# Optimization experiments

Hardware: AMD Instinct MI355X
Metric: run time of the kernel (lower is better)

Reference implementation:

```python
import jax, jax.numpy as jnp
import numpy as np

N_NODES = 50000
N_EDGES = 1600000


def gcn_conv(x, edge_index, W, b):
    """PyG GCNConv: linear transform, add self-loops, symmetric deg^-1/2 norm, scatter-add."""
    n = x.shape[0]
    h = x @ W  # [N, out]
    loop = jnp.arange(n)
    src = jnp.concatenate([edge_index[0], loop])
    dst = jnp.concatenate([edge_index[1], loop])
    ones = jnp.ones(src.shape[0], dtype=h.dtype)
    deg = jax.ops.segment_sum(ones, dst, num_segments=n)  # in-degree incl. self-loop
    dinv = jnp.where(deg > 0, jax.lax.rsqrt(deg), 0.0)
    norm = dinv[src] * dinv[dst]  # [E+N]
    msg = h[src] * norm[:, None]  # gathered, normalized messages
    out = jax.ops.segment_sum(msg, dst, num_segments=n)
    return out + b


def setup_inputs() -> dict:
    key = jax.random.key(0)
    k1, k2, k3, k4 = jax.random.split(key, 4)
    x = jax.random.normal(k1, (N_NODES, 512), dtype=jnp.float32)
    edge_index = jax.random.randint(k2, (2, N_EDGES), 0, N_NODES, dtype=jnp.int64)
    W1 = jax.random.normal(k3, (512, 128), dtype=jnp.float32) * (1.0 / np.sqrt(512))
    b1 = jnp.zeros((128,), dtype=jnp.float32)
    W2 = jax.random.normal(k4, (128, 40), dtype=jnp.float32) * (1.0 / np.sqrt(128))
    b2 = jnp.zeros((40,), dtype=jnp.float32)
    return {"x": x, "edge_index": edge_index, "W1": W1, "b1": b1, "W2": W2, "b2": b2}


def reference(x, edge_index, W1, b1, W2, b2):
    h = gcn_conv(x, edge_index, W1, b1)
    h = jax.nn.relu(h)
    h = gcn_conv(h, edge_index, W2, b2)
    return jax.nn.log_softmax(h, axis=1)
```

## Files before the change

kernel.cpp:

```cpp
#include <hip/hip_runtime.h>
#include <hip/hip_bf16.h>
#include <math.h>


#define FEAT1 512
#define FEAT2 128
#define FEAT3 40

typedef __attribute__((ext_vector_type(8))) short bf16x8;
typedef __attribute__((ext_vector_type(4))) float f32x4;

__device__ __forceinline__ unsigned short f2bf(float f) {
    union { float f; unsigned u; } c; c.f = f;
    unsigned r = c.u + 0x7fff + ((c.u >> 16) & 1);
    return (unsigned short)(r >> 16);
}
__device__ __forceinline__ float bf2f(unsigned v16) {
    union { unsigned u; float f; } c; c.u = v16 << 16;
    return c.f;
}

__global__ void detect_i64_kernel(const int* __restrict__ ei, int* flagp) {
    __shared__ int any;
    if (threadIdx.x == 0) any = 0;
    __syncthreads();
    int v = ei[2 * threadIdx.x + 1];
    if (v != 0) any = 1;
    __syncthreads();
    if (threadIdx.x == 0) *flagp = (any == 0) ? 1 : 0;
}

__device__ __forceinline__ int load_src(const int* ei, long e, long E, int f64) {
    return f64 ? ei[2 * e] : ei[e];
}
__device__ __forceinline__ int load_dst(const int* ei, long e, long E, int f64) {
    return f64 ? ei[2 * E + 2 * e] : ei[E + e];
}

__launch_bounds__(1024)
__global__ void partA_kernel(const int* __restrict__ ei, const int* __restrict__ flagp,
                             int* __restrict__ gbkt, unsigned* __restrict__ part,
                             int bktCap, long E, int NB) {
    __shared__ int hist[256], lbase[256], lcur[256];
    int f64 = *flagp;
    int t = threadIdx.x;
    long chunk = (E + gridDim.x - 1) / gridDim.x;
    long start = (long)blockIdx.x * chunk;
    long end = start + chunk; if (end > E) end = E;
    if (t < 256) { hist[t] = 0; lcur[t] = 0; }
    __syncthreads();

    for (long e0 = start; e0 < end; e0 += 1024) {
        long e = e0 + t;
        if (e < end) {
            int dst = load_dst(ei, e, E, f64);
            atomicAdd(&hist[dst >> 8], 1);
        }
    }
    __syncthreads();
    if (t < NB && hist[t]) lbase[t] = atomicAdd(&gbkt[t], hist[t]);
    __syncthreads();

    for (long e0 = start; e0 < end; e0 += 1024) {
        long e = e0 + t;
        if (e < end) {
            int src = load_src(ei, e, E, f64);
            int dst = load_dst(ei, e, E, f64);
            int bkt = dst >> 8;
            int pos = lbase[bkt] + atomicAdd(&lcur[bkt], 1);
            if (pos < bktCap)
                part[(long)bkt * bktCap + pos] = (unsigned)src | ((unsigned)(dst & 255) << 17);
        }
    }
}

__global__ void bscan_kernel(const int* __restrict__ gbkt, int* __restrict__ bktBase,
                             int* __restrict__ offsets, int NB, int N, int E) {
    __shared__ int s[256];
    int t = threadIdx.x;
    int v = (t < NB) ? gbkt[t] : 0;
    s[t] = v;
    __syncthreads();
    #pragma unroll
    for (int d = 1; d < 256; d <<= 1) {
        int tv = (t >= d) ? s[t - d] : 0;
        __syncthreads();
        s[t] += tv;
        __syncthreads();
    }
    bktBase[t] = s[t] - v;
    if (t == 0) offsets[N] = E;
}

__launch_bounds__(256)
__global__ void partB_kernel(const unsigned* __restrict__ part, int bktCap,
                             const int* __restrict__ gbkt, const int* __restrict__ bktBase,
                             int* __restrict__ offsets, float* __restrict__ dinv,
                             int* __restrict__ col, int N) {
    __shared__ int h[256], sc[256], cur[256];
    int b = blockIdx.x, t = threadIdx.x;
    int n = gbkt[b]; if (n > bktCap) n = bktCap;
    int base = bktBase[b];
    int lo = b << 8;
    const unsigned* p = part + (long)b * bktCap;
    h[t] = 0;
    __syncthreads();
    for (int i = t; i < n; i += 256) atomicAdd(&h[(p[i] >> 17) & 255], 1);
    __syncthreads();
    int cnt = h[t];
    sc[t] = cnt;
    __syncthreads();
    #pragma unroll
    for (int d = 1; d < 256; d <<= 1) {
        int tv = (t >= d) ? sc[t - d] : 0;
        __syncthreads();
        sc[t] += tv;
        __syncthreads();
    }
    int ex = sc[t] - cnt;
    int node = lo + t;
    if (node < N) {
        offsets[node] = base + ex;
        dinv[node] = 1.0f / sqrtf((float)(cnt + 1));
    }
    cur[t] = ex;
    __syncthreads();
    for (int i = t; i < n; i += 256) {
        unsigned u = p[i];
        int r = atomicAdd(&cur[(u >> 17) & 255], 1);
        col[base + r] = u & 0x1FFFF;
    }
}

__global__ void w1bt_kernel(const float* __restrict__ W1, unsigned short* __restrict__ Bt) {
    int n = blockIdx.x;
    for (int k = threadIdx.x; k < FEAT1; k += blockDim.x)
        Bt[(long)n * FEAT1 + k] = f2bf(W1[(long)k * FEAT2 + n]);
}

__global__ void w2bt_kernel(const float* __restrict__ W2, unsigned short* __restrict__ Bt2) {
    int n = blockIdx.x;
    for (int k = threadIdx.x; k < FEAT2; k += blockDim.x)
        Bt2[(long)n * FEAT2 + k] = (n < FEAT3) ? f2bf(W2[(long)k * FEAT3 + n]) : 0;
}

__launch_bounds__(256)
__global__ void gemm1_mfma_kernel(const float* __restrict__ A,
                                  const unsigned short* __restrict__ Bt,
                                  const float* __restrict__ dinv,
                                  unsigned short* __restrict__ C, int M) {
    __shared__ uint4 Asm[256];
    int t = threadIdx.x;
    int m0 = blockIdx.x * 64;
    int w = t >> 6, lane = t & 63;
    int wr = w >> 1, wc = w & 1;
    int quad = lane >> 4, r15 = lane & 15;

    f32x4 acc[2][4];
    #pragma unroll
    for (int mt = 0; mt < 2; mt++)
        #pragma unroll
        for (int nt = 0; nt < 4; nt++) acc[mt][nt] = (f32x4){0.f, 0.f, 0.f, 0.f};

    for (int k0 = 0; k0 < FEAT1; k0 += 32) {
        __syncthreads();
        #pragma unroll
        for (int i = 0; i < 2; i++) {
            int id = t + i * 256;
            int row = id >> 3, q = id & 7;
            int grow = m0 + row;
            float4 v = make_float4(0.f, 0.f, 0.f, 0.f);
            if (grow < M) v = *(const float4*)(A + (long)grow * FEAT1 + k0 + q * 4);
            uint2 p;
            p.x = (unsigned)f2bf(v.x) | ((unsigned)f2bf(v.y) << 16);
            p.y = (unsigned)f2bf(v.z) | ((unsigned)f2bf(v.w) << 16);
            ((uint2*)Asm)[(row >> 4) * 128 + (((row & 15) + ((q >> 1) << 4)) << 1) + (q & 1)] = p;
        }
        __syncthreads();

        bf16x8 af[2];
        #pragma unroll
        for (int mt = 0; mt < 2; mt++)
            af[mt] = ((const bf16x8*)Asm)[(wr * 2 + mt) * 64 + lane];

        #pragma unroll
        for (int nt = 0; nt < 4; nt++) {
            bf16x8 bf = *(const bf16x8*)(Bt + (long)(wc * 64 + nt * 16 + r15) * FEAT1 + k0 + quad * 8);
            acc[0][nt] = __builtin_amdgcn_mfma_f32_16x16x32_bf16(af[0], bf, acc[0][nt], 0, 0, 0);
            acc[1][nt] = __builtin_amdgcn_mfma_f32_16x16x32_bf16(af[1], bf, acc[1][nt], 0, 0, 0);
        }
    }

    #pragma unroll
    for (int mt = 0; mt < 2; mt++) {
        int rb = m0 + wr * 32 + mt * 16 + quad * 4;
        #pragma unroll
        for (int reg = 0; reg < 4; reg++) {
            int row = rb + reg;
            if (row >= M) continue;
            float di = dinv[row];
            #pragma unroll
            for (int nt = 0; nt < 4; nt++) {
                C[(long)row * FEAT2 + wc * 64 + nt * 16 + r15] = f2bf(acc[mt][nt][reg] * di);
            }
        }
    }
}

__launch_bounds__(256)
__global__ void agg1_kernel(const unsigned short* __restrict__ h1s,
                            const int* __restrict__ col, const int* __restrict__ off,
                            const float* __restrict__ dinv, const float* __restrict__ b1,
                            unsigned short* __restrict__ a1, int N) {
    int node = blockIdx.x * 4 + (threadIdx.x >> 6);
    if (node >= N) return;
    int l = threadIdx.x & 63;
    int o0 = off[node], o1 = off[node + 1];
    float ax = 0.f, ay = 0.f;
    for (int base = o0; base < o1; base += 64) {
        int cnt = min(64, o1 - base);
        int myc = (l < cnt) ? col[base + l] : 0;
        int e = 0;
        for (; e + 4 <= cnt; e += 4) {
            int s0 = __shfl(myc, e + 0);
            int s1 = __shfl(myc, e + 1);
            int s2 = __shfl(myc, e + 2);
            int s3 = __shfl(myc, e + 3);
            unsigned p0 = *(const unsigned*)(h1s + (long)s0 * FEAT2 + 2 * l);
            unsigned p1 = *(const unsigned*)(h1s + (long)s1 * FEAT2 + 2 * l);
            unsigned p2 = *(const unsigned*)(h1s + (long)s2 * FEAT2 + 2 * l);
            unsigned p3 = *(const unsigned*)(h1s + (long)s3 * FEAT2 + 2 * l);
            ax += bf2f(p0 & 0xffffu) + bf2f(p1 & 0xffffu) +
                  bf2f(p2 & 0xffffu) + bf2f(p3 & 0xffffu);
            ay += bf2f(p0 >> 16) + bf2f(p1 >> 16) + bf2f(p2 >> 16) + bf2f(p3 >> 16);
        }
        for (; e < cnt; ++e) {
            int s = __shfl(myc, e);
            unsigned p = *(const unsigned*)(h1s + (long)s * FEAT2 + 2 * l);
            ax += bf2f(p & 0xffffu);
            ay += bf2f(p >> 16);
        }
    }
    unsigned pv = *(const unsigned*)(h1s + (long)node * FEAT2 + 2 * l);
    ax += bf2f(pv & 0xffffu);
    ay += bf2f(pv >> 16);
    float di = dinv[node];
    float2 b = *(const float2*)(b1 + 2 * l);
    float vx = ax * di + b.x;
    float vy = ay * di + b.y;
    vx = vx > 0.f ? vx : 0.f;
    vy = vy > 0.f ? vy : 0.f;
    *(unsigned*)(a1 + (long)node * FEAT2 + 2 * l) =
        (unsigned)f2bf(vx) | ((unsigned)f2bf(vy) << 16);
}

__launch_bounds__(256)
__global__ void gemm2_mfma_kernel(const unsigned short* __restrict__ A,
                                  const unsigned short* __restrict__ Bt2,
                                  const float* __restrict__ dinv,
                                  unsigned short* __restrict__ C, int M) {
    int wave = blockIdx.x * (blockDim.x >> 6) + (threadIdx.x >> 6);
    int lane = threadIdx.x & 63;
    int quad = lane >> 4, r15 = lane & 15;
    int row0 = wave * 16;
    if (row0 >= M) return;
    int arow = row0 + r15;
    if (arow >= M) arow = M - 1;

    bf16x8 af[4];
    const unsigned short* ap = A + (long)arow * FEAT2 + quad * 8;
    #pragma unroll
    for (int ks = 0; ks < 4; ks++) af[ks] = *(const bf16x8*)(ap + ks * 32);

    f32x4 acc[3];
    #pragma unroll
    for (int nt = 0; nt < 3; nt++) acc[nt] = (f32x4){0.f, 0.f, 0.f, 0.f};
    #pragma unroll
    for (int ks = 0; ks < 4; ks++) {
        #pragma unroll
        for (int nt = 0; nt < 3; nt++) {
            bf16x8 bf = *(const bf16x8*)(Bt2 + (long)(nt * 16 + r15) * FEAT2 + ks * 32 + quad * 8);
            acc[nt] = __builtin_amdgcn_mfma_f32_16x16x32_bf16(af[ks], bf, acc[nt], 0, 0, 0);
        }
    }

    #pragma unroll
    for (int reg = 0; reg < 4; reg++) {
        int orow = row0 + quad * 4 + reg;
        if (orow >= M) continue;
        float di = dinv[orow];
        #pragma unroll
        for (int nt = 0; nt < 3; nt++) {
            int ocol = nt * 16 + r15;
            if (ocol < FEAT3)
                C[(long)orow * FEAT3 + ocol] = f2bf(acc[nt][reg] * di);
        }
    }
}

__launch_bounds__(256)
__global__ void agg2_lsm_kernel(const unsigned short* __restrict__ h2s,
                                const int* __restrict__ col, const int* __restrict__ off,
                                const float* __restrict__ dinv, const float* __restrict__ b2,
                                float* __restrict__ out, int N) {
    int node = blockIdx.x * 4 + (threadIdx.x >> 6);
    if (node >= N) return;
    int l = threadIdx.x & 63;
    bool act = l < FEAT3 / 2;
    int o0 = off[node], o1 = off[node + 1];
    float ax = 0.f, ay = 0.f;
    for (int base = o0; base < o1; base += 64) {
        int cnt = min(64, o1 - base);
        int myc = (l < cnt) ? col[base + l] : 0;
        int e = 0;
        for (; e + 4 <= cnt; e += 4) {
            int s0 = __shfl(myc, e + 0);
            int s1 = __shfl(myc, e + 1);
            int s2 = __shfl(myc, e + 2);
            int s3 = __shfl(myc, e + 3);
            if (act) {
                unsigned p0 = *(const unsigned*)(h2s + (long)s0 * FEAT3 + 2 * l);
                unsigned p1 = *(const unsigned*)(h2s + (long)s1 * FEAT3 + 2 * l);
                unsigned p2 = *(const unsigned*)(h2s + (long)s2 * FEAT3 + 2 * l);
                unsigned p3 = *(const unsigned*)(h2s + (long)s3 * FEAT3 + 2 * l);
                ax += bf2f(p0 & 0xffffu) + bf2f(p1 & 0xffffu) +
                      bf2f(p2 & 0xffffu) + bf2f(p3 & 0xffffu);
                ay += bf2f(p0 >> 16) + bf2f(p1 >> 16) + bf2f(p2 >> 16) + bf2f(p3 >> 16);
            }
        }
        for (; e < cnt; ++e) {
            int s = __shfl(myc, e);
            if (act) {
                unsigned p = *(const unsigned*)(h2s + (long)s * FEAT3 + 2 * l);
                ax += bf2f(p & 0xffffu);
                ay += bf2f(p >> 16);
            }
        }
    }
    float vx = -INFINITY, vy = -INFINITY;
    if (act) {
        unsigned pv = *(const unsigned*)(h2s + (long)node * FEAT3 + 2 * l);
        float di = dinv[node];
        float2 b = *(const float2*)(b2 + 2 * l);
        vx = (ax + bf2f(pv & 0xffffu)) * di + b.x;
        vy = (ay + bf2f(pv >> 16)) * di + b.y;
    }
    float m = fmaxf(vx, vy);
    #pragma unroll
    for (int o = 32; o >= 1; o >>= 1) m = fmaxf(m, __shfl_xor(m, o));
    float e = act ? (expf(vx - m) + expf(vy - m)) : 0.f;
    #pragma unroll
    for (int o = 32; o >= 1; o >>= 1) e += __shfl_xor(e, o);
    float ls = logf(e);
    if (act) {
        *(float2*)(out + (long)node * FEAT3 + 2 * l) = make_float2(vx - m - ls, vy - m - ls);
    }
}

extern "C" void kernel_launch(void* const* d_in, const int* in_sizes, int n_in,
                              void* d_out, int out_size, void* d_ws, size_t ws_size,
                              hipStream_t stream) {
    const float* x  = (const float*)d_in[0];
    const int*   ei = (const int*)d_in[1];
    const float* W1 = (const float*)d_in[2];
    const float* b1 = (const float*)d_in[3];
    const float* W2 = (const float*)d_in[4];
    const float* b2 = (const float*)d_in[5];
    float* out = (float*)d_out;

    const int  N = in_sizes[0] / FEAT1;
    const long E = in_sizes[1] / 2;

    char* ws = (char*)d_ws;
    size_t off = 0;
    auto alloc = [&](size_t bytes) -> void* {
        off = (off + 255) & ~(size_t)255;
        void* p = ws + off;
        off += bytes;
        return p;
    };
    const int NB = (N + 255) >> 8;
    const int bktCap = (int)(E / NB) + 1024;
    int*   offsets = (int*)alloc((size_t)(N + 1) * 4);
    float* dinv    = (float*)alloc((size_t)N * 4);
    int*   col     = (int*)alloc((size_t)E * 4);
    unsigned short* h1s = (unsigned short*)alloc((size_t)N * FEAT2 * 2);
    unsigned short* a1  = (unsigned short*)alloc((size_t)N * FEAT2 * 2);
    unsigned short* h2s = (unsigned short*)alloc((size_t)N * FEAT3 * 2);
    unsigned short* Bt  = (unsigned short*)alloc((size_t)FEAT2 * FEAT1 * 2);
    unsigned short* Bt2 = (unsigned short*)alloc((size_t)48 * FEAT2 * 2);
    unsigned* part = (unsigned*)alloc((size_t)NB * bktCap * 4);
    int*   gbkt    = (int*)alloc(256 * 4);
    int*   bktBase = (int*)alloc(256 * 4);
    int*   flagp   = (int*)alloc(4);

    detect_i64_kernel<<<1, 256, 0, stream>>>(ei, flagp);
    hipMemsetAsync(gbkt, 0, 256 * 4, stream);
    partA_kernel<<<256, 1024, 0, stream>>>(ei, flagp, gbkt, part, bktCap, E, NB);
    bscan_kernel<<<1, 256, 0, stream>>>(gbkt, bktBase, offsets, NB, N, (int)E);
    partB_kernel<<<NB, 256, 0, stream>>>(part, bktCap, gbkt, bktBase, offsets, dinv, col, N);

    w1bt_kernel<<<FEAT2, 256, 0, stream>>>(W1, Bt);
    w2bt_kernel<<<48, 128, 0, stream>>>(W2, Bt2);
    gemm1_mfma_kernel<<<(N + 63) / 64, 256, 0, stream>>>(x, Bt, dinv, h1s, N);
    agg1_kernel<<<(N + 3) / 4, 256, 0, stream>>>(h1s, col, offsets, dinv, b1, a1, N);
    gemm2_mfma_kernel<<<(N / 16 + 3) / 4, 256, 0, stream>>>(a1, Bt2, dinv, h2s, N);
    agg2_lsm_kernel<<<(N + 3) / 4, 256, 0, stream>>>(h2s, col, offsets, dinv, b2, out, N);
}
```

Before: 344.3 us.

## Replace shared-memory GEMM1 with register-resident per-wave 16-row MFMA kernel

The first GEMM now has each wave own 16 rows and all 128 output columns. Its A fragments are loaded straight from global memory into registers in two K halves, with the second half prefetched while the first half's MFMAs run. This removes the LDS staging and __syncthreads barriers, and lets x be streamed with more loads in flight. In exchange, register pressure is much higher and the B matrix is reloaded by every wave instead of being shared across waves in a block.

```diff
diff --git a/kernel.cpp b/kernel.cpp
--- a/kernel.cpp
+++ b/kernel.cpp
@@ -18,6 +18,15 @@
 __device__ __forceinline__ float bf2f(unsigned v16) {
     union { unsigned u; float f; } c; c.u = v16 << 16;
     return c.f;
+}
+
+__device__ __forceinline__ bf16x8 pack_bf8(f32x4 a, f32x4 b) {
+    bf16x8 r;
+    r[0] = (short)f2bf(a[0]); r[1] = (short)f2bf(a[1]);
+    r[2] = (short)f2bf(a[2]); r[3] = (short)f2bf(a[3]);
+    r[4] = (short)f2bf(b[0]); r[5] = (short)f2bf(b[1]);
+    r[6] = (short)f2bf(b[2]); r[7] = (short)f2bf(b[3]);
+    return r;
 }
 
 __global__ void detect_i64_kernel(const int* __restrict__ ei, int* flagp) {
@@ -145,65 +154,70 @@
 }
 
 __launch_bounds__(256)
-__global__ void gemm1_mfma_kernel(const float* __restrict__ A,
-                                  const unsigned short* __restrict__ Bt,
-                                  const float* __restrict__ dinv,
-                                  unsigned short* __restrict__ C, int M) {
-    __shared__ uint4 Asm[256];
-    int t = threadIdx.x;
-    int m0 = blockIdx.x * 64;
-    int w = t >> 6, lane = t & 63;
-    int wr = w >> 1, wc = w & 1;
+__global__ void gemm1_reg_kernel(const float* __restrict__ A,
+                                 const unsigned short* __restrict__ Bt,
+                                 const float* __restrict__ dinv,
+                                 unsigned short* __restrict__ C, int M) {
+    int wave = blockIdx.x * 4 + (threadIdx.x >> 6);
+    int lane = threadIdx.x & 63;
     int quad = lane >> 4, r15 = lane & 15;
-
-    f32x4 acc[2][4];
-    #pragma unroll
-    for (int mt = 0; mt < 2; mt++)
+    int row0 = wave * 16;
+    if (row0 >= M) return;
+    int arow = row0 + r15;
+    if (arow >= M) arow = M - 1;
+    const float* ap = A + (long)arow * FEAT1 + quad * 8;
+    const unsigned short* bp = Bt + (long)r15 * FEAT1 + quad * 8;
+
+    f32x4 raw[16];
+    #pragma unroll
+    for (int ks = 0; ks < 8; ks++) {
+        raw[2 * ks]     = *(const f32x4*)(ap + ks * 32);
+        raw[2 * ks + 1] = *(const f32x4*)(ap + ks * 32 + 4);
+    }
+
+    f32x4 acc[8];
+    #pragma unroll
+    for (int nt = 0; nt < 8; nt++) acc[nt] = (f32x4){0.f, 0.f, 0.f, 0.f};
+
+    bf16x8 af[8];
+    #pragma unroll
+    for (int ks = 0; ks < 8; ks++) af[ks] = pack_bf8(raw[2 * ks], raw[2 * ks + 1]);
+
+    #pragma unroll
+    for (int ks = 0; ks < 8; ks++) {
+        raw[2 * ks]     = *(const f32x4*)(ap + 256 + ks * 32);
+        raw[2 * ks + 1] = *(const f32x4*)(ap + 256 + ks * 32 + 4);
+    }
+
+    #pragma unroll
+    for (int ks = 0; ks < 8; ks++) {
         #pragma unroll
-        for (int nt = 0; nt < 4; nt++) acc[mt][nt] = (f32x4){0.f, 0.f, 0.f, 0.f};
-
-    for (int k0 = 0; k0 < FEAT1; k0 += 32) {
-        __syncthreads();
+        for (int nt = 0; nt < 8; nt++) {
+            bf16x8 bfrag = *(const bf16x8*)(bp + (long)nt * 16 * FEAT1 + ks * 32);
+            acc[nt] = __builtin_amdgcn_mfma_f32_16x16x32_bf16(af[ks], bfrag, acc[nt], 0, 0, 0);
+        }
+    }
+
+    #pragma unroll
+    for (int ks = 0; ks < 8; ks++) af[ks] = pack_bf8(raw[2 * ks], raw[2 * ks + 1]);
+
+    #pragma unroll
+    for (int ks = 0; ks < 8; ks++) {
         #pragma unroll
-        for (int i = 0; i < 2; i++) {
-            int id = t + i * 256;
-            int row = id >> 3, q = id & 7;
-            int grow = m0 + row;
-            float4 v = make_float4(0.f, 0.f, 0.f, 0.f);
-            if (grow < M) v = *(const float4*)(A + (long)grow * FEAT1 + k0 + q * 4);
-            uint2 p;
-            p.x = (unsigned)f2bf(v.x) | ((unsigned)f2bf(v.y) << 16);
-            p.y = (unsigned)f2bf(v.z) | ((unsigned)f2bf(v.w) << 16);
-            ((uint2*)Asm)[(row >> 4) * 128 + (((row & 15) + ((q >> 1) << 4)) << 1) + (q & 1)] = p;
-        }
-        __syncthreads();
-
-        bf16x8 af[2];
+        for (int nt = 0; nt < 8; nt++) {
+            bf16x8 bfrag = *(const bf16x8*)(bp + (long)nt * 16 * FEAT1 + 256 + ks * 32);
+            acc[nt] = __builtin_amdgcn_mfma_f32_16x16x32_bf16(af[ks], bfrag, acc[nt], 0, 0, 0);
+        }
+    }
+
+    #pragma unroll
+    for (int reg = 0; reg < 4; reg++) {
+        int orow = row0 + quad * 4 + reg;
+        if (orow >= M) continue;
+        float di = dinv[orow];
         #pragma unroll
-        for (int mt = 0; mt < 2; mt++)
-            af[mt] = ((const bf16x8*)Asm)[(wr * 2 + mt) * 64 + lane];
-
-        #pragma unroll
-        for (int nt = 0; nt < 4; nt++) {
-            bf16x8 bf = *(const bf16x8*)(Bt + (long)(wc * 64 + nt * 16 + r15) * FEAT1 + k0 + quad * 8);
-            acc[0][nt] = __builtin_amdgcn_mfma_f32_16x16x32_bf16(af[0], bf, acc[0][nt], 0, 0, 0);
-            acc[1][nt] = __builtin_amdgcn_mfma_f32_16x16x32_bf16(af[1], bf, acc[1][nt], 0, 0, 0);
-        }
-    }
-
-    #pragma unroll
-    for (int mt = 0; mt < 2; mt++) {
-        int rb = m0 + wr * 32 + mt * 16 + quad * 4;
-        #pragma unroll
-        for (int reg = 0; reg < 4; reg++) {
-            int row = rb + reg;
-            if (row >= M) continue;
-            float di = dinv[row];
-            #pragma unroll
-            for (int nt = 0; nt < 4; nt++) {
-                C[(long)row * FEAT2 + wc * 64 + nt * 16 + r15] = f2bf(acc[mt][nt][reg] * di);
-            }
-        }
+        for (int nt = 0; nt < 8; nt++)
+            C[(long)orow * FEAT2 + nt * 16 + r15] = f2bf(acc[nt][reg] * di);
     }
 }
 
@@ -402,7 +416,10 @@
 
     w1bt_kernel<<<FEAT2, 256, 0, stream>>>(W1, Bt);
     w2bt_kernel<<<48, 128, 0, stream>>>(W2, Bt2);
-    gemm1_mfma_kernel<<<(N + 63) / 64, 256, 0, stream>>>(x, Bt, dinv, h1s, N);
+    {
+        int waves = (N + 15) / 16;
+        gemm1_reg_kernel<<<(waves + 3) / 4, 256, 0, stream>>>(x, Bt, dinv, h1s, N);
+    }
     agg1_kernel<<<(N + 3) / 4, 256, 0, stream>>>(h1s, col, offsets, dinv, b1, a1, N);
     gemm2_mfma_kernel<<<(N / 16 + 3) / 4, 256, 0, stream>>>(a1, Bt2, dinv, h2s, N);
     agg2_lsm_kernel<<<(N + 3) / 4, 256, 0, stream>>>(h2s, col, offsets, dinv, b2, out, N);
```

Result: slower. 368.4 us (+7.0%).
